# Optimization experiments

Measured on AMD Instinct MI355X. Metric: run time of the kernel, lower is better.

The kernel has to match this reference:

```python
import jax, jax.numpy as jnp
import numpy as np

HIDDEN = 2048
INPUT = 2048
BATCH = 4096


def setup_inputs() -> dict:
    key = jax.random.key(0)
    ks = jax.random.split(key, 7)
    x = jax.random.normal(ks[0], (BATCH, INPUT), dtype=jnp.float32)
    h = jax.random.normal(ks[1], (BATCH, HIDDEN), dtype=jnp.float32)
    c = jax.random.normal(ks[2], (BATCH, HIDDEN), dtype=jnp.float32)
    # learned parameters (RandomNormal init stddev=0.05 analogue; scale irrelevant for correctness)
    w_ih = jax.random.normal(ks[3], (4, INPUT, HIDDEN), dtype=jnp.float32) * 0.05
    w_hh = jax.random.normal(ks[4], (4, HIDDEN, HIDDEN), dtype=jnp.float32) * 0.05
    b_ih = jax.random.normal(ks[5], (4, HIDDEN), dtype=jnp.float32) * 0.05
    b_hh = jax.random.normal(ks[6], (4, HIDDEN), dtype=jnp.float32) * 0.05
    return {"x": x, "h": h, "c": c, "w_ih": w_ih, "w_hh": w_hh, "b_ih": b_ih, "b_hh": b_hh}


def reference(x, h, c, w_ih, w_hh, b_ih, b_hh):
    # gates: [4, B, H] = x @ w_ih[g] and h @ w_hh[g], batched over gate dim g
    gates = (
        jnp.einsum("bi,gih->gbh", x, w_ih)
        + jnp.einsum("bh,ghk->gbk", h, w_hh)
        + (b_ih + b_hh)[:, None, :]
    )
    ingate = jax.nn.sigmoid(gates[0])
    forgetgate = jax.nn.sigmoid(gates[1])
    cellgate = jnp.tanh(gates[2])
    outgate = jax.nn.sigmoid(gates[3])
    c_new = forgetgate * c + ingate * cellgate
    h_new = outgate * jnp.tanh(c_new)
    return (h_new, c_new)
```

## Files before the change

### kernel.cpp

```cpp
#include <hip/hip_runtime.h>

#define BATCH  4096
#define HIDDEN 2048
#define INPUT  2048
#define KDIM   4096
#define NDIM   8192
#define BM 256
#define BN 256
#define BK 64
#define NT (KDIM / BK)

typedef __attribute__((ext_vector_type(8))) short short8;
typedef __attribute__((ext_vector_type(4))) float float4v;


__device__ __forceinline__ unsigned short f2bf(float f) {
    union { float f; unsigned u; } v; v.f = f;
    unsigned r = v.u + 0x7FFFu + ((v.u >> 16) & 1u);
    return (unsigned short)(r >> 16);
}

__device__ __forceinline__ void gl2lds16(const unsigned short* g, unsigned short* l) {
    __builtin_amdgcn_global_load_lds(
        (const __attribute__((address_space(1))) unsigned int*)g,
        (__attribute__((address_space(3))) unsigned int*)l,
        16, 0, 0);
}

__device__ __forceinline__ float sigm(float x) {
    return 1.0f / (1.0f + __expf(-x));
}
__device__ __forceinline__ float tanh_fast(float x) {
    return 2.0f / (1.0f + __expf(-2.0f * x)) - 1.0f;
}

__device__ __forceinline__ void fence_bar() {
    asm volatile("" ::: "memory");
    __builtin_amdgcn_s_barrier();
    asm volatile("" ::: "memory");
}


__global__ void pack_x_kernel(const float* __restrict__ x, const float* __restrict__ h,
                              unsigned short* __restrict__ Xb) {
    int idx = blockIdx.x * 256 + threadIdx.x;
    int b  = idx >> 9;
    int ko = idx & 511;
    const float* src = (ko < 256) ? (x + (size_t)b * INPUT  + (size_t)ko * 8)
                                  : (h + (size_t)b * HIDDEN + (size_t)(ko - 256) * 8);
    float4 v0 = *(const float4*)(src);
    float4 v1 = *(const float4*)(src + 4);
    union { unsigned short us[8]; uint4 v; } o;
    o.us[0] = f2bf(v0.x); o.us[1] = f2bf(v0.y); o.us[2] = f2bf(v0.z); o.us[3] = f2bf(v0.w);
    o.us[4] = f2bf(v1.x); o.us[5] = f2bf(v1.y); o.us[6] = f2bf(v1.z); o.us[7] = f2bf(v1.w);
    *(uint4*)(Xb + (size_t)b * KDIM + (size_t)ko * 8) = o.v;
}


__global__ void pack_w_kernel(const float* __restrict__ w_ih, const float* __restrict__ w_hh,
                              unsigned short* __restrict__ Wt) {
    __shared__ unsigned short tile[32][136];
    const int k0 = blockIdx.x * 128;
    const int j0 = blockIdx.y * 32;
    const int g  = blockIdx.z;
    const float* src = (k0 < INPUT)
        ? (w_ih + (size_t)g * INPUT  * HIDDEN + (size_t)k0 * HIDDEN + j0)
        : (w_hh + (size_t)g * HIDDEN * HIDDEN + (size_t)(k0 - INPUT) * HIDDEN + j0);

    const int tid = threadIdx.x;
    const int jl  = (tid & 7) * 4;
    const int kl  = (tid >> 3) * 2;
#pragma unroll
    for (int p = 0; p < 2; ++p) {
        const int k = kl + p * 64;
        float4 v0 = *(const float4*)(src + (size_t)k * HIDDEN + jl);
        float4 v1 = *(const float4*)(src + (size_t)(k + 1) * HIDDEN + jl);
        unsigned p0 = (unsigned)f2bf(v0.x) | ((unsigned)f2bf(v1.x) << 16);
        unsigned p1 = (unsigned)f2bf(v0.y) | ((unsigned)f2bf(v1.y) << 16);
        unsigned p2 = (unsigned)f2bf(v0.z) | ((unsigned)f2bf(v1.z) << 16);
        unsigned p3 = (unsigned)f2bf(v0.w) | ((unsigned)f2bf(v1.w) << 16);
        *(unsigned*)&tile[jl + 0][kl + p * 64] = p0;
        *(unsigned*)&tile[jl + 1][kl + p * 64] = p1;
        *(unsigned*)&tile[jl + 2][kl + p * 64] = p2;
        *(unsigned*)&tile[jl + 3][kl + p * 64] = p3;
    }
    __syncthreads();

#pragma unroll
    for (int p = 0; p < 2; ++p) {
        const int cch = tid + p * 256;
        const int j   = cch >> 4;
        const int k8  = cch & 15;
        uint4 v = *(const uint4*)&tile[j][k8 * 8];
        *(uint4*)(Wt + (size_t)(4 * (j0 + j) + g) * KDIM + k0 + k8 * 8) = v;
    }
}


__global__ __launch_bounds__(512, 1)
void gemm_kernel(const unsigned short* __restrict__ A,
                 const unsigned short* __restrict__ B,
                 const float* __restrict__ c,
                 const float* __restrict__ b_ih,
                 const float* __restrict__ b_hh,
                 float* __restrict__ out) {
    extern __shared__ unsigned short lds[];
    unsigned short* cA = lds;
    unsigned short* nA = lds + 16384;
    unsigned short* cB = lds + 32768;
    unsigned short* nB = lds + 49152;

    const int tid  = threadIdx.x;
    const int wid  = tid >> 6;
    const int lane = tid & 63;
    const int ln   = lane & 15;
    const int kq   = lane >> 4;
    const int wmr  = (wid >> 2) * 128;
    const int wnr  = (wid & 3) * 64;

    const int nwgx = NDIM / BN;
    const int L    = blockIdx.y * nwgx + blockIdx.x;
    const int cpx  = (nwgx * (BATCH / BM)) >> 3;
    const int Ls   = (L & 7) * cpx + (L >> 3);
    const int m0   = (Ls / nwgx) * BM;
    const int n0   = (Ls % nwgx) * BN;

    const int srow  = tid >> 3;
    const int scol8 = (tid & 7) ^ (srow & 7);
    const unsigned short* gA[4];
    const unsigned short* gB[4];
#pragma unroll
    for (int cN = 0; cN < 4; ++cN) {
        gA[cN] = A + (size_t)(m0 + cN * 64 + srow) * KDIM + scol8 * 8;
        gB[cN] = B + (size_t)(n0 + cN * 64 + srow) * KDIM + scol8 * 8;
    }
    const int dOff = tid * 8;

    const int abase = (wmr + ln) * 64;
    const int bbase = (wnr + ln) * 64;
    const int sk0 = ((0 + kq) ^ (ln & 7)) * 8;
    const int sk1 = ((4 + kq) ^ (ln & 7)) * 8;

    float4v acc[8][4];
#pragma unroll
    for (int i = 0; i < 8; ++i)
#pragma unroll
        for (int j = 0; j < 4; ++j)
            acc[i][j] = (float4v){0.f, 0.f, 0.f, 0.f};

#define STAGE_A(cN) gl2lds16(gA[cN] + konext, nA + (cN) * 4096 + dOff)
#define STAGE_B(cN) gl2lds16(gB[cN] + konext, nB + (cN) * 4096 + dOff)

    {
#pragma unroll
        for (int cN = 0; cN < 4; ++cN) gl2lds16(gB[cN], cB + cN * 4096 + dOff);
#pragma unroll
        for (int cN = 0; cN < 4; ++cN) gl2lds16(gA[cN], cA + cN * 4096 + dOff);
    }

    short8 bf[4][2];

    for (int T = 0; T < NT; ++T) {
        const bool last = (T == NT - 1);
        const int konext = (T + 1) * BK;

        if (!last) {
            STAGE_B(0); STAGE_B(1); STAGE_B(2); STAGE_B(3);
            STAGE_A(0); STAGE_A(1); STAGE_A(2); STAGE_A(3);
            asm volatile("s_waitcnt vmcnt(8)" ::: "memory");
        } else {
            asm volatile("s_waitcnt vmcnt(0)" ::: "memory");
        }
        fence_bar();

#pragma unroll
        for (int ni = 0; ni < 4; ++ni) {
            bf[ni][0] = *(const short8*)(cB + bbase + ni * 1024 + sk0);
            bf[ni][1] = *(const short8*)(cB + bbase + ni * 1024 + sk1);
        }
#pragma unroll
        for (int ph = 0; ph < 4; ++ph) {
            short8 a00 = *(const short8*)(cA + abase + (2 * ph) * 1024 + sk0);
            short8 a01 = *(const short8*)(cA + abase + (2 * ph) * 1024 + sk1);
            short8 a10 = *(const short8*)(cA + abase + (2 * ph + 1) * 1024 + sk0);
            short8 a11 = *(const short8*)(cA + abase + (2 * ph + 1) * 1024 + sk1);
            __builtin_amdgcn_s_setprio(1);
#pragma unroll
            for (int ni = 0; ni < 4; ++ni)
                acc[2 * ph][ni] = __builtin_amdgcn_mfma_f32_16x16x32_bf16(a00, bf[ni][0], acc[2 * ph][ni], 0, 0, 0);
#pragma unroll
            for (int ni = 0; ni < 4; ++ni)
                acc[2 * ph + 1][ni] = __builtin_amdgcn_mfma_f32_16x16x32_bf16(a10, bf[ni][0], acc[2 * ph + 1][ni], 0, 0, 0);
#pragma unroll
            for (int ni = 0; ni < 4; ++ni)
                acc[2 * ph][ni] = __builtin_amdgcn_mfma_f32_16x16x32_bf16(a01, bf[ni][1], acc[2 * ph][ni], 0, 0, 0);
#pragma unroll
            for (int ni = 0; ni < 4; ++ni)
                acc[2 * ph + 1][ni] = __builtin_amdgcn_mfma_f32_16x16x32_bf16(a11, bf[ni][1], acc[2 * ph + 1][ni], 0, 0, 0);
            __builtin_amdgcn_s_setprio(0);
        }

        fence_bar();

        unsigned short* t0 = cA; cA = nA; nA = t0;
        unsigned short* t1 = cB; cB = nB; nB = t1;
    }
#undef STAGE_A
#undef STAGE_B

    const int qg = lane & 3;
    const int tq = (lane & 15) >> 2;
    const int jb = (n0 >> 2) + (wnr >> 2);
    const size_t HB = (size_t)BATCH * HIDDEN;

    float bia[4][4];
#pragma unroll
    for (int ni = 0; ni < 4; ++ni) {
        const int jgq = jb + ni * 4 + tq;
        bia[ni][0] = b_ih[jgq]              + b_hh[jgq];
        bia[ni][1] = b_ih[HIDDEN + jgq]     + b_hh[HIDDEN + jgq];
        bia[ni][2] = b_ih[2 * HIDDEN + jgq] + b_hh[2 * HIDDEN + jgq];
        bia[ni][3] = b_ih[3 * HIDDEN + jgq] + b_hh[3 * HIDDEN + jgq];
    }

#pragma unroll
    for (int mi = 0; mi < 8; ++mi) {
        float fgv[4], pv[4], ogv[4];
#pragma unroll
        for (int ni = 0; ni < 4; ++ni) {
            float4v v = acc[mi][ni];
            float t1 = __shfl_xor((qg & 1) ? v[0] : v[1], 1);
            float t2 = __shfl_xor((qg & 1) ? v[2] : v[3], 1);
            v[0] = (qg & 1) ? t1 : v[0];
            v[1] = (qg & 1) ? v[1] : t1;
            v[2] = (qg & 1) ? t2 : v[2];
            v[3] = (qg & 1) ? v[3] : t2;
            float t3 = __shfl_xor((qg & 2) ? v[0] : v[2], 2);
            float t4 = __shfl_xor((qg & 2) ? v[1] : v[3], 2);
            v[0] = (qg & 2) ? t3 : v[0];
            v[1] = (qg & 2) ? t4 : v[1];
            v[2] = (qg & 2) ? v[2] : t3;
            v[3] = (qg & 2) ? v[3] : t4;

            const float ig = sigm(v[0] + bia[ni][0]);
            const float fg = sigm(v[1] + bia[ni][1]);
            const float cg = tanh_fast(v[2] + bia[ni][2]);
            const float og = sigm(v[3] + bia[ni][3]);
            fgv[ni] = fg;
            pv[ni]  = ig * cg;
            ogv[ni] = og;
        }
#define TRANS_T(a)                                                        \
        {                                                                 \
            float u1 = __shfl_xor((tq & 1) ? a[0] : a[1], 4);             \
            float u2 = __shfl_xor((tq & 1) ? a[2] : a[3], 4);             \
            a[0] = (tq & 1) ? u1 : a[0];                                  \
            a[1] = (tq & 1) ? a[1] : u1;                                  \
            a[2] = (tq & 1) ? u2 : a[2];                                  \
            a[3] = (tq & 1) ? a[3] : u2;                                  \
            float u3 = __shfl_xor((tq & 2) ? a[0] : a[2], 8);             \
            float u4 = __shfl_xor((tq & 2) ? a[1] : a[3], 8);             \
            a[0] = (tq & 2) ? u3 : a[0];                                  \
            a[2] = (tq & 2) ? a[2] : u3;                                  \
            a[1] = (tq & 2) ? u4 : a[1];                                  \
            a[3] = (tq & 2) ? a[3] : u4;                                  \
        }
        TRANS_T(fgv);
        TRANS_T(pv);
        TRANS_T(ogv);
#undef TRANS_T

        const int row = m0 + wmr + mi * 16 + kq * 4 + qg;
        const int jcol = jb + 4 * tq;
        const float4 cv = *(const float4*)(c + (size_t)row * HIDDEN + jcol);
        float4 hn4, cn4;
        {
            const float cn0 = fgv[0] * cv.x + pv[0];
            const float cn1 = fgv[1] * cv.y + pv[1];
            const float cn2 = fgv[2] * cv.z + pv[2];
            const float cn3 = fgv[3] * cv.w + pv[3];
            cn4.x = cn0; cn4.y = cn1; cn4.z = cn2; cn4.w = cn3;
            hn4.x = ogv[0] * tanh_fast(cn0);
            hn4.y = ogv[1] * tanh_fast(cn1);
            hn4.z = ogv[2] * tanh_fast(cn2);
            hn4.w = ogv[3] * tanh_fast(cn3);
        }
        *(float4*)(out + (size_t)row * HIDDEN + jcol)      = hn4;
        *(float4*)(out + HB + (size_t)row * HIDDEN + jcol) = cn4;
    }
}


extern "C" void kernel_launch(void* const* d_in, const int* in_sizes, int n_in,
                              void* d_out, int out_size, void* d_ws, size_t ws_size,
                              hipStream_t stream) {
    const float* x    = (const float*)d_in[0];
    const float* h    = (const float*)d_in[1];
    const float* c    = (const float*)d_in[2];
    const float* w_ih = (const float*)d_in[3];
    const float* w_hh = (const float*)d_in[4];
    const float* b_ih = (const float*)d_in[5];
    const float* b_hh = (const float*)d_in[6];
    float* out = (float*)d_out;

    const size_t XB_BYTES = (size_t)BATCH * KDIM * 2;
    unsigned short* Xb = (unsigned short*)d_ws;
    unsigned short* Wt = (unsigned short*)((char*)d_ws + XB_BYTES);

    hipLaunchKernelGGL(pack_x_kernel, dim3((size_t)BATCH * KDIM / 8 / 256), dim3(256), 0, stream,
                       x, h, Xb);
    hipLaunchKernelGGL(pack_w_kernel, dim3(KDIM / 128, HIDDEN / 32, 4), dim3(256), 0, stream,
                       w_ih, w_hh, Wt);
    hipLaunchKernelGGL(gemm_kernel, dim3(NDIM / BN, BATCH / BM), dim3(512), 131072, stream,
                       Xb, Wt, c, b_ih, b_hh, out);
}
```

Baseline: 488.8 us.

## Double-buffer A fragments in registers and drop XCD-aware block remapping

Software-pipelines the A-fragment LDS reads so the next phase's fragments load while the current phase's MFMAs issue, which should hide LDS latency inside the k-tile. It also removes the workgroup index swizzle that grouped tiles per XCD and uses plain blockIdx mapping instead. That can reduce L2 reuse across XCDs, and the extra fragment registers raise register pressure.

Measured after the change: 482.5 us. About the same (-1.3%).

```diff
diff --git a/kernel.cpp b/kernel.cpp
--- a/kernel.cpp
+++ b/kernel.cpp
@@ -117,13 +117,8 @@
     const int kq   = lane >> 4;
     const int wmr  = (wid >> 2) * 128;
     const int wnr  = (wid & 3) * 64;
-
-    const int nwgx = NDIM / BN;
-    const int L    = blockIdx.y * nwgx + blockIdx.x;
-    const int cpx  = (nwgx * (BATCH / BM)) >> 3;
-    const int Ls   = (L & 7) * cpx + (L >> 3);
-    const int m0   = (Ls / nwgx) * BM;
-    const int n0   = (Ls % nwgx) * BN;
+    const int m0   = blockIdx.y * BM;
+    const int n0   = blockIdx.x * BN;
 
     const int srow  = tid >> 3;
     const int scol8 = (tid & 7) ^ (srow & 7);
@@ -150,6 +145,8 @@
 
 #define STAGE_A(cN) gl2lds16(gA[cN] + konext, nA + (cN) * 4096 + dOff)
 #define STAGE_B(cN) gl2lds16(gB[cN] + konext, nB + (cN) * 4096 + dOff)
+#define RD_A(ph, r) (*(const short8*)(cA + abase + (2 * (ph) + ((r) >> 1)) * 1024 \
+                                      + (((r) & 1) ? sk1 : sk0)))
 
     {
 #pragma unroll
@@ -158,7 +155,8 @@
         for (int cN = 0; cN < 4; ++cN) gl2lds16(gA[cN], cA + cN * 4096 + dOff);
     }
 
-    short8 bf[4][2];
+    short8 bfv[4][2];
+    short8 afr[2][4];
 
     for (int T = 0; T < NT; ++T) {
         const bool last = (T == NT - 1);
@@ -174,29 +172,36 @@
         fence_bar();
 
 #pragma unroll
+        for (int r = 0; r < 4; ++r) afr[0][r] = RD_A(0, r);
+#pragma unroll
         for (int ni = 0; ni < 4; ++ni) {
-            bf[ni][0] = *(const short8*)(cB + bbase + ni * 1024 + sk0);
-            bf[ni][1] = *(const short8*)(cB + bbase + ni * 1024 + sk1);
+            bfv[ni][0] = *(const short8*)(cB + bbase + ni * 1024 + sk0);
+            bfv[ni][1] = *(const short8*)(cB + bbase + ni * 1024 + sk1);
         }
 #pragma unroll
         for (int ph = 0; ph < 4; ++ph) {
-            short8 a00 = *(const short8*)(cA + abase + (2 * ph) * 1024 + sk0);
-            short8 a01 = *(const short8*)(cA + abase + (2 * ph) * 1024 + sk1);
-            short8 a10 = *(const short8*)(cA + abase + (2 * ph + 1) * 1024 + sk0);
-            short8 a11 = *(const short8*)(cA + abase + (2 * ph + 1) * 1024 + sk1);
+            const int cur = ph & 1;
+            if (ph < 3) {
+#pragma unroll
+                for (int r = 0; r < 4; ++r) afr[cur ^ 1][r] = RD_A(ph + 1, r);
+            }
             __builtin_amdgcn_s_setprio(1);
 #pragma unroll
             for (int ni = 0; ni < 4; ++ni)
-                acc[2 * ph][ni] = __builtin_amdgcn_mfma_f32_16x16x32_bf16(a00, bf[ni][0], acc[2 * ph][ni], 0, 0, 0);
+                acc[2 * ph][ni] = __builtin_amdgcn_mfma_f32_16x16x32_bf16(
+                    afr[cur][0], bfv[ni][0], acc[2 * ph][ni], 0, 0, 0);
 #pragma unroll
             for (int ni = 0; ni < 4; ++ni)
-                acc[2 * ph + 1][ni] = __builtin_amdgcn_mfma_f32_16x16x32_bf16(a10, bf[ni][0], acc[2 * ph + 1][ni], 0, 0, 0);
+                acc[2 * ph + 1][ni] = __builtin_amdgcn_mfma_f32_16x16x32_bf16(
+                    afr[cur][2], bfv[ni][0], acc[2 * ph + 1][ni], 0, 0, 0);
 #pragma unroll
             for (int ni = 0; ni < 4; ++ni)
-                acc[2 * ph][ni] = __builtin_amdgcn_mfma_f32_16x16x32_bf16(a01, bf[ni][1], acc[2 * ph][ni], 0, 0, 0);
+                acc[2 * ph][ni] = __builtin_amdgcn_mfma_f32_16x16x32_bf16(
+                    afr[cur][1], bfv[ni][1], acc[2 * ph][ni], 0, 0, 0);
 #pragma unroll
             for (int ni = 0; ni < 4; ++ni)
-                acc[2 * ph + 1][ni] = __builtin_amdgcn_mfma_f32_16x16x32_bf16(a11, bf[ni][1], acc[2 * ph + 1][ni], 0, 0, 0);
+                acc[2 * ph + 1][ni] = __builtin_amdgcn_mfma_f32_16x16x32_bf16(
+                    afr[cur][3], bfv[ni][1], acc[2 * ph + 1][ni], 0, 0, 0);
             __builtin_amdgcn_s_setprio(0);
         }
 
@@ -207,6 +212,7 @@
     }
 #undef STAGE_A
 #undef STAGE_B
+#undef RD_A
 
     const int qg = lane & 3;
     const int tq = (lane & 15) >> 2;
```
